# Kernel tuning notes

Hardware: AMD Instinct MI355X
Metric: run time of the kernel (lower is better)

The kernel has to match this reference:

```python
import jax, jax.numpy as jnp
import numpy as np

B, T, C, H = 2, 2048, 1024, 16
D = C // H  # head_dim = 64


def setup_inputs() -> dict:
    key = jax.random.key(0)
    ks = jax.random.split(key, 5)
    x = jax.random.normal(ks[0], (B, T, C), dtype=jnp.float32)
    # fused QKV projection: Linear(C, 3C)
    W_qkv = jax.random.normal(ks[1], (C, 3 * C), dtype=jnp.float32) / np.sqrt(C)
    b_qkv = jax.random.normal(ks[2], (3 * C,), dtype=jnp.float32) * 0.02
    # output projection: Linear(C, C)
    W_proj = jax.random.normal(ks[3], (C, C), dtype=jnp.float32) / np.sqrt(C)
    b_proj = jax.random.normal(ks[4], (C,), dtype=jnp.float32) * 0.02
    return {"x": x, "W_qkv": W_qkv, "b_qkv": b_qkv, "W_proj": W_proj, "b_proj": b_proj}


def reference(x, W_qkv, b_qkv, W_proj, b_proj):
    # fused QKV projection
    qkv = jnp.einsum("btc,cd->btd", x, W_qkv) + b_qkv  # [B,T,3C]
    q, k, v = jnp.split(qkv, 3, axis=-1)
    # [B,T,C] -> [B,H,T,D]
    def to_heads(t):
        return t.reshape(B, T, H, D).transpose(0, 2, 1, 3)
    q, k, v = to_heads(q), to_heads(k), to_heads(v)
    # causal scaled dot-product attention (SDPA default scale = 1/sqrt(head_dim))
    scale = 1.0 / np.sqrt(D).astype(np.float32)
    scores = jnp.einsum("bhqd,bhkd->bhqk", q, k) * scale  # [B,H,T,T]
    causal = jnp.tril(jnp.ones((T, T), dtype=bool))
    scores = jnp.where(causal, scores, jnp.finfo(scores.dtype).min)
    attn = jax.nn.softmax(scores, axis=-1)
    out = jnp.einsum("bhqk,bhkd->bhqd", attn, v)  # [B,H,T,D]
    out = out.transpose(0, 2, 1, 3).reshape(B, T, C)
    # output projection
    return jnp.einsum("btc,cd->btd", out, W_proj) + b_proj
```

## Files before the change

### kernel.cpp

```cpp
#include <hip/hip_runtime.h>
#include <hip/hip_bf16.h>

typedef __attribute__((ext_vector_type(8))) __bf16 bf16x8;
typedef __attribute__((ext_vector_type(8))) short short8;
typedef __attribute__((ext_vector_type(4))) float f32x4;
typedef __attribute__((ext_vector_type(16))) float f32x16;
typedef __attribute__((ext_vector_type(4))) short sh4;

typedef __attribute__((address_space(1))) void GVoid;
typedef __attribute__((address_space(3))) void LVoid;

#define NEGBIG (-1e30f)
#define SCL 0.18033688011112042f

constexpr int TT = 2048, CC = 1024, HH = 16, DD = 64, C3 = 3072;

__device__ __forceinline__ unsigned short f2bf(float f) {
  unsigned int i = __float_as_uint(f);
  return (unsigned short)((i + 0x7FFFu + ((i >> 16) & 1u)) >> 16);
}
__device__ __forceinline__ void async16(const void* g, void* l) {
  __builtin_amdgcn_global_load_lds((GVoid*)g, (LVoid*)l, 16, 0, 0);
}

__global__ __launch_bounds__(256) void cvt_bf16(
    const float* __restrict__ in, unsigned short* __restrict__ out, int n8)
{
  const int i = blockIdx.x * 256 + threadIdx.x;
  if (i >= n8) return;
  const float* p = in + (size_t)i * 8;
  f32x4 a = *(const f32x4*)p, b = *(const f32x4*)(p + 4);
  sh4 r0, r1;
  ((unsigned short*)&r0)[0] = f2bf(a[0]); ((unsigned short*)&r0)[1] = f2bf(a[1]);
  ((unsigned short*)&r0)[2] = f2bf(a[2]); ((unsigned short*)&r0)[3] = f2bf(a[3]);
  ((unsigned short*)&r1)[0] = f2bf(b[0]); ((unsigned short*)&r1)[1] = f2bf(b[1]);
  ((unsigned short*)&r1)[2] = f2bf(b[2]); ((unsigned short*)&r1)[3] = f2bf(b[3]);
  *(sh4*)(out + (size_t)i * 8) = r0;
  *(sh4*)(out + (size_t)i * 8 + 4) = r1;
}

__global__ __launch_bounds__(256) void transpose_cvt(
    const float* __restrict__ in, unsigned short* __restrict__ out, int R, int Cd)
{
  __shared__ __align__(16) unsigned short tile[64 * 72];
  const int r0 = blockIdx.y * 64, c0 = blockIdx.x * 64;
  const int tid = threadIdx.x;
#pragma unroll
  for (int r = 0; r < 2; ++r) {
    const int elem = r * 2048 + tid * 8;
    const int ii = elem >> 6, jj = elem & 63;
    const float* p = in + (size_t)(r0 + ii) * Cd + c0 + jj;
    f32x4 a = *(const f32x4*)p, b = *(const f32x4*)(p + 4);
    short8 v;
    ((unsigned short*)&v)[0] = f2bf(a[0]); ((unsigned short*)&v)[1] = f2bf(a[1]);
    ((unsigned short*)&v)[2] = f2bf(a[2]); ((unsigned short*)&v)[3] = f2bf(a[3]);
    ((unsigned short*)&v)[4] = f2bf(b[0]); ((unsigned short*)&v)[5] = f2bf(b[1]);
    ((unsigned short*)&v)[6] = f2bf(b[2]); ((unsigned short*)&v)[7] = f2bf(b[3]);
    *(short8*)&tile[ii * 72 + jj] = v;
  }
  __syncthreads();
#pragma unroll
  for (int r = 0; r < 2; ++r) {
    const int elem = r * 2048 + tid * 8;
    const int jj = elem >> 6, ii0 = elem & 63;
    short8 v;
#pragma unroll
    for (int e = 0; e < 8; ++e) ((unsigned short*)&v)[e] = tile[(ii0 + e) * 72 + jj];
    *(short8*)&out[(size_t)(c0 + jj) * R + r0 + ii0] = v;
  }
}

template <int MODE>
__global__ __launch_bounds__(256) void gemm_bt(
    const unsigned short* __restrict__ A,
    const unsigned short* __restrict__ Bt,
    const float* __restrict__ bias,
    void* __restrict__ Cp, unsigned short* __restrict__ Vt,
    int M, int N, int K, int lda)
{
  __shared__ __align__(16) unsigned short sA[2][128 * 32];
  __shared__ __align__(16) unsigned short sB[2][128 * 32];
  const int tid = threadIdx.x;
  const int w = tid >> 6, l = tid & 63, ln = l & 15, quad = l >> 4;
  const int wm = w >> 1, wn = w & 1;
  const int m0 = blockIdx.y * 128, n0 = blockIdx.x * 128;
  f32x4 acc[4][4] = {};

  const int elem0 = tid * 8;
  const int ar0 = elem0 >> 5, ac0 = elem0 & 31;
  const int ar1 = (2048 + elem0) >> 5, ac1 = ac0;

  async16(A  + (size_t)(m0 + ar0) * lda + ac0, &sA[0][w * 512]);
  async16(Bt + (size_t)(n0 + ar0) * K   + ac0, &sB[0][w * 512]);
  async16(A  + (size_t)(m0 + ar1) * lda + ac1, &sA[0][2048 + w * 512]);
  async16(Bt + (size_t)(n0 + ar1) * K   + ac1, &sB[0][2048 + w * 512]);
  __syncthreads();

  int buf = 0;
  for (int k0 = 0; k0 < K; k0 += 32, buf ^= 1) {
    if (k0 + 32 < K) {
      const int nb = buf ^ 1, kn = k0 + 32;
      async16(A  + (size_t)(m0 + ar0) * lda + kn + ac0, &sA[nb][w * 512]);
      async16(Bt + (size_t)(n0 + ar0) * K   + kn + ac0, &sB[nb][w * 512]);
      async16(A  + (size_t)(m0 + ar1) * lda + kn + ac1, &sA[nb][2048 + w * 512]);
      async16(Bt + (size_t)(n0 + ar1) * K   + kn + ac1, &sB[nb][2048 + w * 512]);
    }

    bf16x8 af[4], bfr[4];
#pragma unroll
    for (int i = 0; i < 4; i++)
      af[i] = *(const bf16x8*)&sA[buf][(wm * 64 + i * 16 + ln) * 32 + quad * 8];
#pragma unroll
    for (int j = 0; j < 4; j++)
      bfr[j] = *(const bf16x8*)&sB[buf][(wn * 64 + j * 16 + ln) * 32 + quad * 8];
#pragma unroll
    for (int i = 0; i < 4; i++)
#pragma unroll
      for (int j = 0; j < 4; j++)
        acc[i][j] = __builtin_amdgcn_mfma_f32_16x16x32_bf16(af[i], bfr[j], acc[i][j], 0, 0, 0);

    __syncthreads();
  }

  float bj[4];
#pragma unroll
  for (int j = 0; j < 4; j++) bj[j] = bias[n0 + wn * 64 + j * 16 + ln];

#pragma unroll
  for (int i = 0; i < 4; i++) {
#pragma unroll
    for (int j = 0; j < 4; j++) {
      const int gn = n0 + wn * 64 + j * 16 + ln;
      if (MODE == 0 && gn >= 2048) {
        const int hh = (gn >> 6) & 15, dd = gn & 63;
        const int gm0 = m0 + wm * 64 + i * 16 + quad * 4;
        const int bb = gm0 >> 11, t0 = gm0 & 2047;
        sh4 rv;
#pragma unroll
        for (int g = 0; g < 4; ++g)
          ((unsigned short*)&rv)[g] = f2bf(acc[i][j][g] + bj[j]);
        *(sh4*)&Vt[((size_t)((bb * HH + hh) * DD + dd)) * TT + t0] = rv;
      } else {
#pragma unroll
        for (int g = 0; g < 4; ++g) {
          const int gm = m0 + wm * 64 + i * 16 + quad * 4 + g;
          float v = acc[i][j][g] + bj[j];
          if (MODE == 0) {
            if (gn < 1024) v *= SCL;
            ((unsigned short*)Cp)[(size_t)gm * 2048 + gn] = f2bf(v);
          } else {
            ((float*)Cp)[(size_t)gm * N + gn] = v;
          }
        }
      }
    }
  }
}

__global__ __launch_bounds__(256) void gemm_n64(
    const unsigned short* __restrict__ A,
    const unsigned short* __restrict__ Bt,
    const float* __restrict__ bias,
    float* __restrict__ Cp, int M, int N, int K, int lda)
{
  __shared__ __align__(16) unsigned short sA[2][128 * 32];
  __shared__ __align__(16) unsigned short sB[2][64 * 32];
  const int tid = threadIdx.x;
  const int w = tid >> 6, l = tid & 63, ln = l & 15, quad = l >> 4;
  const int wm = w >> 1, wn = w & 1;
  const int m0 = blockIdx.y * 128, n0 = blockIdx.x * 64;
  f32x4 acc[4][2] = {};

  const int elem0 = tid * 8;
  const int ar0 = elem0 >> 5, ac0 = elem0 & 31;
  const int ar1 = (2048 + elem0) >> 5, ac1 = ac0;

  async16(A  + (size_t)(m0 + ar0) * lda + ac0, &sA[0][w * 512]);
  async16(A  + (size_t)(m0 + ar1) * lda + ac1, &sA[0][2048 + w * 512]);
  async16(Bt + (size_t)(n0 + ar0) * K   + ac0, &sB[0][w * 512]);
  __syncthreads();

  int buf = 0;
  for (int k0 = 0; k0 < K; k0 += 32, buf ^= 1) {
    if (k0 + 32 < K) {
      const int nb = buf ^ 1, kn = k0 + 32;
      async16(A  + (size_t)(m0 + ar0) * lda + kn + ac0, &sA[nb][w * 512]);
      async16(A  + (size_t)(m0 + ar1) * lda + kn + ac1, &sA[nb][2048 + w * 512]);
      async16(Bt + (size_t)(n0 + ar0) * K   + kn + ac0, &sB[nb][w * 512]);
    }

    bf16x8 af[4], bfr[2];
#pragma unroll
    for (int i = 0; i < 4; i++)
      af[i] = *(const bf16x8*)&sA[buf][(wm * 64 + i * 16 + ln) * 32 + quad * 8];
#pragma unroll
    for (int j = 0; j < 2; j++)
      bfr[j] = *(const bf16x8*)&sB[buf][(wn * 32 + j * 16 + ln) * 32 + quad * 8];
#pragma unroll
    for (int i = 0; i < 4; i++)
#pragma unroll
      for (int j = 0; j < 2; j++)
        acc[i][j] = __builtin_amdgcn_mfma_f32_16x16x32_bf16(af[i], bfr[j], acc[i][j], 0, 0, 0);

    __syncthreads();
  }

  float bj[2];
#pragma unroll
  for (int j = 0; j < 2; j++) bj[j] = bias[n0 + wn * 32 + j * 16 + ln];

#pragma unroll
  for (int i = 0; i < 4; i++)
#pragma unroll
    for (int g = 0; g < 4; ++g) {
      const int gm = m0 + wm * 64 + i * 16 + quad * 4 + g;
#pragma unroll
      for (int j = 0; j < 2; j++) {
        const int gn = n0 + wn * 32 + j * 16 + ln;
        Cp[(size_t)gm * N + gn] = acc[i][j][g] + bj[j];
      }
    }
}

__global__ __launch_bounds__(512) void attn2g(
    unsigned short* __restrict__ QK, const unsigned short* __restrict__ Vt)
{
  __shared__ __align__(16) unsigned short kt[2][2][64 * 72];
  __shared__ __align__(16) unsigned short vt[2][3][64 * 72];
  __shared__ float Ox[4][2][16][64];
  __shared__ float Lx[4][64];
  const int pair = blockIdx.x, bh = blockIdx.y;
  const int b = bh >> 4, h = bh & 15;
  const int tid = threadIdx.x;
  const int grp = tid >> 8, gtid = tid & 255;
  const int wg = (tid >> 6) & 3, l = tid & 63;
  const int c = l & 31, h2 = l >> 5;
  unsigned short*       Qp = QK + (size_t)b * TT * 2048 + h * DD;
  const unsigned short* Kp = QK + (size_t)b * TT * 2048 + CC + h * DD;
  const unsigned short* Vh = Vt + (size_t)bh * DD * TT;
  const int si0 = gtid >> 3, so = (gtid & 7) * 8;

  for (int ph = 0; ph < 2; ++ph) {
    const int qt = ph ? 15 - pair : pair;
    const int qbase = qt * 128 + wg * 32;
    const int qm = qbase + c - 4 * h2;
    bf16x8 qv[4];
#pragma unroll
    for (int ds = 0; ds < 4; ++ds)
      qv[ds] = *(const bf16x8*)&Qp[(size_t)(qbase + c) * 2048 + ds * 16 + h2 * 8];

    f32x16 oacc[2] = {};
    bf16x8 pA[4] = {};
    float lsum = 0.0f;
    const int nslot = qt + 1;
    int vm1 = 2, v0 = 0, vp1 = 1;

    __syncthreads();
#pragma unroll
    for (int r = 0; r < 2; ++r) {
      const int si = si0 + 32 * r;
      *(short8*)&kt[grp][0][si * 72 + so] =
          *(const short8*)&Kp[(size_t)(grp * 64 + si) * 2048 + so];
      *(short8*)&vt[grp][0][si * 72 + so] =
          *(const short8*)&Vh[(size_t)si * TT + grp * 64 + so];
    }
    __syncthreads();

    for (int slot = 0; slot < nslot; ++slot) {
      const int kb = 2 * slot + grp;
      const int ck = slot & 1;
      short8 pk[2], pv[2];
      if (slot + 1 < nslot) {
        const int kbn = kb + 2;
#pragma unroll
        for (int r = 0; r < 2; ++r) {
          const int si = si0 + 32 * r;
          pk[r] = *(const short8*)&Kp[(size_t)(kbn * 64 + si) * 2048 + so];
          pv[r] = *(const short8*)&Vh[(size_t)si * TT + kbn * 64 + so];
        }
      }
      const bool qk_act = (kb * 64 <= qbase + 31);
      f32x16 sacc[2];
      if (qk_act) {
#pragma unroll
        for (int kg = 0; kg < 2; ++kg) {
          f32x16 sa = {};
#pragma unroll
          for (int ds = 0; ds < 4; ++ds) {
            bf16x8 kf = *(const bf16x8*)&kt[grp][ck][(kg * 32 + c) * 72 + ds * 16 + h2 * 8];
            sa = __builtin_amdgcn_mfma_f32_32x32x16_bf16(kf, qv[ds], sa, 0, 0, 0);
          }
          sacc[kg] = sa;
        }
      }
      if (slot > 0 && (kb - 2) * 64 <= qbase + 31) {
        const unsigned short* vp = vt[grp][vm1];
#pragma unroll
        for (int dg = 0; dg < 2; ++dg)
#pragma unroll
          for (int ks = 0; ks < 4; ++ks) {
            bf16x8 vf = *(const bf16x8*)&vp[(dg * 32 + c) * 72 + ks * 16 + h2 * 8];
            oacc[dg] = __builtin_amdgcn_mfma_f32_32x32x16_bf16(pA[ks], vf, oacc[dg], 0, 0, 0);
          }
      }
      if (qk_act) {
        const bool need_mask = (kb * 64 + 63 > qbase);
        float pe[2][16];
#pragma unroll
        for (int kg = 0; kg < 2; ++kg)
#pragma unroll
          for (int rr = 0; rr < 16; ++rr) {
            float sv = sacc[kg][rr];
            if (need_mask) {
              const int krel = kb * 64 + kg * 32 + (rr & 3) + 8 * (rr >> 2);
              if (krel > qm) sv = NEGBIG;
            }
            float e;
            asm("v_exp_f32 %0, %1" : "=v"(e) : "v"(sv));
            pe[kg][rr] = e;
            lsum += e;
          }
        unsigned W0[2][4], W1[2][4];
#pragma unroll
        for (int kg = 0; kg < 2; ++kg)
#pragma unroll
          for (int r4 = 0; r4 < 4; ++r4) {
            asm("v_cvt_pk_bf16_f32 %0, %1, %2"
                : "=v"(W0[kg][r4]) : "v"(pe[kg][4 * r4 + 0]), "v"(pe[kg][4 * r4 + 1]));
            asm("v_cvt_pk_bf16_f32 %0, %1, %2"
                : "=v"(W1[kg][r4]) : "v"(pe[kg][4 * r4 + 2]), "v"(pe[kg][4 * r4 + 3]));
          }
#pragma unroll
        for (int ks = 0; ks < 4; ++ks) {
          const int kg = ks >> 1, sel = ks & 1;
          unsigned a0 = W0[kg][2 * sel], b0 = W0[kg][2 * sel + 1];
          unsigned a1 = W1[kg][2 * sel], b1 = W1[kg][2 * sel + 1];
          asm("v_permlane32_swap_b32 %0, %1" : "+v"(a0), "+v"(b0));
          asm("v_permlane32_swap_b32 %0, %1" : "+v"(a1), "+v"(b1));
          unsigned wds[4] = {a0, a1, b0, b1};
          pA[ks] = *(const bf16x8*)wds;
        }
      }
      if (slot + 1 < nslot) {
#pragma unroll
        for (int r = 0; r < 2; ++r) {
          const int si = si0 + 32 * r;
          *(short8*)&kt[grp][1 - ck][si * 72 + so] = pk[r];
          *(short8*)&vt[grp][vp1][si * 72 + so] = pv[r];
        }
      }
      __syncthreads();
      const int t_ = vm1; vm1 = v0; v0 = vp1; vp1 = t_;
    }
    const int kb_last = 2 * qt + grp;
    if (kb_last * 64 <= qbase + 31) {
      const unsigned short* vp = vt[grp][vm1];
#pragma unroll
      for (int dg = 0; dg < 2; ++dg)
#pragma unroll
        for (int ks = 0; ks < 4; ++ks) {
          bf16x8 vf = *(const bf16x8*)&vp[(dg * 32 + c) * 72 + ks * 16 + h2 * 8];
          oacc[dg] = __builtin_amdgcn_mfma_f32_32x32x16_bf16(pA[ks], vf, oacc[dg], 0, 0, 0);
        }
    }
    lsum += __shfl_xor(lsum, 32);
    if (grp == 1) {
#pragma unroll
      for (int dg = 0; dg < 2; ++dg)
#pragma unroll
        for (int rr = 0; rr < 16; ++rr) Ox[wg][dg][rr][l] = oacc[dg][rr];
      Lx[wg][l] = lsum;
    }
    __syncthreads();
    if (grp == 0) {
      const float inv = 1.0f / (lsum + Lx[wg][l]);
#pragma unroll
      for (int dg = 0; dg < 2; ++dg)
#pragma unroll
        for (int rr = 0; rr < 16; ++rr) oacc[dg][rr] += Ox[wg][dg][rr][l];
#pragma unroll
      for (int rr = 0; rr < 16; ++rr) {
        const int q_rel = (rr & 3) + 8 * (rr >> 2) + 4 * h2;
        const float iq = __shfl(inv, q_rel);
        const size_t trow = qbase + q_rel;
#pragma unroll
        for (int dg = 0; dg < 2; ++dg)
          Qp[trow * 2048 + dg * 32 + c] = f2bf(oacc[dg][rr] * iq);
      }
    }
  }
}

extern "C" void kernel_launch(void* const* d_in, const int* in_sizes, int n_in,
                              void* d_out, int out_size, void* d_ws, size_t ws_size,
                              hipStream_t stream)
{
  (void)in_sizes; (void)n_in; (void)out_size; (void)ws_size;
  const float* x     = (const float*)d_in[0];
  const float* Wqkv  = (const float*)d_in[1];
  const float* bqkv  = (const float*)d_in[2];
  const float* Wproj = (const float*)d_in[3];
  const float* bproj = (const float*)d_in[4];

  unsigned short* QK     = (unsigned short*)d_ws;
  unsigned short* WqkvT  = QK + (size_t)4096 * 2048;
  unsigned short* WprojT = WqkvT;
  unsigned short* Vt = (unsigned short*)d_out;
  unsigned short* xb = Vt + (size_t)32 * 64 * 2048;

  cvt_bf16<<<dim3(4096 * 1024 / 8 / 256), 256, 0, stream>>>(x, xb, 4096 * 1024 / 8);
  transpose_cvt<<<dim3(C3 / 64, CC / 64), 256, 0, stream>>>(Wqkv, WqkvT, CC, C3);
  gemm_bt<0><<<dim3(C3 / 128, 4096 / 128), 256, 0, stream>>>(
      xb, WqkvT, bqkv, QK, Vt, 4096, C3, CC, CC);
  transpose_cvt<<<dim3(CC / 64, CC / 64), 256, 0, stream>>>(Wproj, WprojT, CC, CC);
  attn2g<<<dim3(8, 2 * HH), 512, 0, stream>>>(QK, Vt);
  gemm_n64<<<dim3(CC / 64, 4096 / 128), 256, 0, stream>>>(
      QK, WprojT, bproj, (float*)d_out, 4096, CC, CC, 2048);
}
```

Before: 180.4 us.

## Split attention key blocks across four wave groups and swizzle GEMM block order

The attention kernel now runs 1024 threads per block, with four groups of waves each handling every fourth key block. Each group keeps its own double-buffered K/V tiles, replacing the two-group scheme that used a triple-buffered, software-pipelined P·V step. Partial outputs and row sums are reduced through shared memory that reuses the K/V buffers. Both GEMMs also remap block IDs with an 8-way swizzle, intended to improve L2 locality. The change adds more parallelism per attention tile, but costs a larger shared-memory footprint, only one block per CU, and a bigger final reduction.

```diff
diff --git a/kernel.cpp b/kernel.cpp
--- a/kernel.cpp
+++ b/kernel.cpp
@@ -83,7 +83,11 @@
   const int tid = threadIdx.x;
   const int w = tid >> 6, l = tid & 63, ln = l & 15, quad = l >> 4;
   const int wm = w >> 1, wn = w & 1;
-  const int m0 = blockIdx.y * 128, n0 = blockIdx.x * 128;
+  const int lid = blockIdx.y * gridDim.x + blockIdx.x;
+  const int per = (gridDim.x * gridDim.y) >> 3;
+  const int swz = (lid & 7) * per + (lid >> 3);
+  const int bx = swz / gridDim.y, by = swz % gridDim.y;
+  const int m0 = by * 128, n0 = bx * 128;
   f32x4 acc[4][4] = {};
 
   const int elem0 = tid * 8;
@@ -168,7 +172,11 @@
   const int tid = threadIdx.x;
   const int w = tid >> 6, l = tid & 63, ln = l & 15, quad = l >> 4;
   const int wm = w >> 1, wn = w & 1;
-  const int m0 = blockIdx.y * 128, n0 = blockIdx.x * 64;
+  const int lid = blockIdx.y * gridDim.x + blockIdx.x;
+  const int per = (gridDim.x * gridDim.y) >> 3;
+  const int swz = (lid & 7) * per + (lid >> 3);
+  const int bx = swz / gridDim.y, by = swz % gridDim.y;
+  const int m0 = by * 128, n0 = bx * 64;
   f32x4 acc[4][2] = {};
 
   const int elem0 = tid * 8;
@@ -222,23 +230,24 @@
     }
 }
 
-__global__ __launch_bounds__(512) void attn2g(
+__global__ __launch_bounds__(1024, 1) void attn4g(
     unsigned short* __restrict__ QK, const unsigned short* __restrict__ Vt)
 {
-  __shared__ __align__(16) unsigned short kt[2][2][64 * 72];
-  __shared__ __align__(16) unsigned short vt[2][3][64 * 72];
-  __shared__ float Ox[4][2][16][64];
-  __shared__ float Lx[4][64];
+  __shared__ __align__(16) unsigned short smem[73728];
   const int pair = blockIdx.x, bh = blockIdx.y;
   const int b = bh >> 4, h = bh & 15;
   const int tid = threadIdx.x;
-  const int grp = tid >> 8, gtid = tid & 255;
-  const int wg = (tid >> 6) & 3, l = tid & 63;
+  const int wid = tid >> 6, grp = wid >> 2, wg = wid & 3, l = tid & 63;
   const int c = l & 31, h2 = l >> 5;
+  const int gtid = tid & 255;
   unsigned short*       Qp = QK + (size_t)b * TT * 2048 + h * DD;
   const unsigned short* Kp = QK + (size_t)b * TT * 2048 + CC + h * DD;
   const unsigned short* Vh = Vt + (size_t)bh * DD * TT;
   const int si0 = gtid >> 3, so = (gtid & 7) * 8;
+  unsigned short* kt0 = smem + grp * 2 * 4608;
+  unsigned short* vt0 = smem + 36864 + grp * 2 * 4608;
+  float* Ms  = (float*)smem;
+  float* Lxp = (float*)smem + 24576;
 
   for (int ph = 0; ph < 2; ++ph) {
     const int qt = ph ? 15 - pair : pair;
@@ -250,60 +259,47 @@
       qv[ds] = *(const bf16x8*)&Qp[(size_t)(qbase + c) * 2048 + ds * 16 + h2 * 8];
 
     f32x16 oacc[2] = {};
-    bf16x8 pA[4] = {};
     float lsum = 0.0f;
-    const int nslot = qt + 1;
-    int vm1 = 2, v0 = 0, vp1 = 1;
+    const int kbmax = 2 * qt + 1;
+    const int nslot = (qt + 2) >> 1;
 
     __syncthreads();
-#pragma unroll
-    for (int r = 0; r < 2; ++r) {
-      const int si = si0 + 32 * r;
-      *(short8*)&kt[grp][0][si * 72 + so] =
-          *(const short8*)&Kp[(size_t)(grp * 64 + si) * 2048 + so];
-      *(short8*)&vt[grp][0][si * 72 + so] =
-          *(const short8*)&Vh[(size_t)si * TT + grp * 64 + so];
+    if (grp <= kbmax) {
+#pragma unroll
+      for (int r = 0; r < 2; ++r) {
+        const int si = si0 + 32 * r;
+        *(short8*)&kt0[si * 72 + so] = *(const short8*)&Kp[(size_t)(grp * 64 + si) * 2048 + so];
+        *(short8*)&vt0[si * 72 + so] = *(const short8*)&Vh[(size_t)si * TT + grp * 64 + so];
+      }
     }
     __syncthreads();
 
     for (int slot = 0; slot < nslot; ++slot) {
-      const int kb = 2 * slot + grp;
+      const int kb = 4 * slot + grp;
       const int ck = slot & 1;
+      const bool pref = (kb + 4 <= kbmax);
       short8 pk[2], pv[2];
-      if (slot + 1 < nslot) {
-        const int kbn = kb + 2;
+      if (pref) {
 #pragma unroll
         for (int r = 0; r < 2; ++r) {
           const int si = si0 + 32 * r;
-          pk[r] = *(const short8*)&Kp[(size_t)(kbn * 64 + si) * 2048 + so];
-          pv[r] = *(const short8*)&Vh[(size_t)si * TT + kbn * 64 + so];
-        }
-      }
-      const bool qk_act = (kb * 64 <= qbase + 31);
-      f32x16 sacc[2];
-      if (qk_act) {
+          pk[r] = *(const short8*)&Kp[(size_t)((kb + 4) * 64 + si) * 2048 + so];
+          pv[r] = *(const short8*)&Vh[(size_t)si * TT + (kb + 4) * 64 + so];
+        }
+      }
+      const bool act = (kb * 64 <= qbase + 31);
+      if (act) {
+        f32x16 sacc[2];
 #pragma unroll
         for (int kg = 0; kg < 2; ++kg) {
           f32x16 sa = {};
 #pragma unroll
           for (int ds = 0; ds < 4; ++ds) {
-            bf16x8 kf = *(const bf16x8*)&kt[grp][ck][(kg * 32 + c) * 72 + ds * 16 + h2 * 8];
+            bf16x8 kf = *(const bf16x8*)&kt0[ck * 4608 + (kg * 32 + c) * 72 + ds * 16 + h2 * 8];
             sa = __builtin_amdgcn_mfma_f32_32x32x16_bf16(kf, qv[ds], sa, 0, 0, 0);
           }
           sacc[kg] = sa;
         }
-      }
-      if (slot > 0 && (kb - 2) * 64 <= qbase + 31) {
-        const unsigned short* vp = vt[grp][vm1];
-#pragma unroll
-        for (int dg = 0; dg < 2; ++dg)
-#pragma unroll
-          for (int ks = 0; ks < 4; ++ks) {
-            bf16x8 vf = *(const bf16x8*)&vp[(dg * 32 + c) * 72 + ks * 16 + h2 * 8];
-            oacc[dg] = __builtin_amdgcn_mfma_f32_32x32x16_bf16(pA[ks], vf, oacc[dg], 0, 0, 0);
-          }
-      }
-      if (qk_act) {
         const bool need_mask = (kb * 64 + 63 > qbase);
         float pe[2][16];
 #pragma unroll
@@ -330,6 +326,7 @@
             asm("v_cvt_pk_bf16_f32 %0, %1, %2"
                 : "=v"(W1[kg][r4]) : "v"(pe[kg][4 * r4 + 2]), "v"(pe[kg][4 * r4 + 3]));
           }
+        bf16x8 pA[4];
 #pragma unroll
         for (int ks = 0; ks < 4; ++ks) {
           const int kg = ks >> 1, sel = ks & 1;
@@ -340,44 +337,50 @@
           unsigned wds[4] = {a0, a1, b0, b1};
           pA[ks] = *(const bf16x8*)wds;
         }
-      }
-      if (slot + 1 < nslot) {
+#pragma unroll
+        for (int dg = 0; dg < 2; ++dg)
+#pragma unroll
+          for (int ks = 0; ks < 4; ++ks) {
+            bf16x8 vf = *(const bf16x8*)&vt0[ck * 4608 + (dg * 32 + c) * 72 + ks * 16 + h2 * 8];
+            oacc[dg] = __builtin_amdgcn_mfma_f32_32x32x16_bf16(pA[ks], vf, oacc[dg], 0, 0, 0);
+          }
+      }
+      if (pref) {
 #pragma unroll
         for (int r = 0; r < 2; ++r) {
           const int si = si0 + 32 * r;
-          *(short8*)&kt[grp][1 - ck][si * 72 + so] = pk[r];
-          *(short8*)&vt[grp][vp1][si * 72 + so] = pv[r];
+          *(short8*)&kt0[(1 - ck) * 4608 + si * 72 + so] = pk[r];
+          *(short8*)&vt0[(1 - ck) * 4608 + si * 72 + so] = pv[r];
         }
       }
       __syncthreads();
-      const int t_ = vm1; vm1 = v0; v0 = vp1; vp1 = t_;
-    }
-    const int kb_last = 2 * qt + grp;
-    if (kb_last * 64 <= qbase + 31) {
-      const unsigned short* vp = vt[grp][vm1];
+    }
+    lsum += __shfl_xor(lsum, 32);
+    if (grp != 0) {
+      const int base = ((grp - 1) * 4 + wg) * 2048;
 #pragma unroll
       for (int dg = 0; dg < 2; ++dg)
 #pragma unroll
-        for (int ks = 0; ks < 4; ++ks) {
-          bf16x8 vf = *(const bf16x8*)&vp[(dg * 32 + c) * 72 + ks * 16 + h2 * 8];
-          oacc[dg] = __builtin_amdgcn_mfma_f32_32x32x16_bf16(pA[ks], vf, oacc[dg], 0, 0, 0);
-        }
-    }
-    lsum += __shfl_xor(lsum, 32);
-    if (grp == 1) {
-#pragma unroll
-      for (int dg = 0; dg < 2; ++dg)
-#pragma unroll
-        for (int rr = 0; rr < 16; ++rr) Ox[wg][dg][rr][l] = oacc[dg][rr];
-      Lx[wg][l] = lsum;
+        for (int rr = 0; rr < 16; ++rr)
+          Ms[base + (dg * 16 + rr) * 64 + l] = oacc[dg][rr];
+      Lxp[((grp - 1) * 4 + wg) * 64 + l] = lsum;
     }
     __syncthreads();
     if (grp == 0) {
-      const float inv = 1.0f / (lsum + Lx[wg][l]);
+      float lt = lsum;
+#pragma unroll
+      for (int g = 1; g < 4; ++g) lt += Lxp[((g - 1) * 4 + wg) * 64 + l];
+      const float inv = 1.0f / lt;
 #pragma unroll
       for (int dg = 0; dg < 2; ++dg)
 #pragma unroll
-        for (int rr = 0; rr < 16; ++rr) oacc[dg][rr] += Ox[wg][dg][rr][l];
+        for (int rr = 0; rr < 16; ++rr) {
+          float o = oacc[dg][rr];
+#pragma unroll
+          for (int g = 1; g < 4; ++g)
+            o += Ms[((g - 1) * 4 + wg) * 2048 + (dg * 16 + rr) * 64 + l];
+          oacc[dg][rr] = o;
+        }
 #pragma unroll
       for (int rr = 0; rr < 16; ++rr) {
         const int q_rel = (rr & 3) + 8 * (rr >> 2) + 4 * h2;
@@ -413,7 +416,7 @@
   gemm_bt<0><<<dim3(C3 / 128, 4096 / 128), 256, 0, stream>>>(
       xb, WqkvT, bqkv, QK, Vt, 4096, C3, CC, CC);
   transpose_cvt<<<dim3(CC / 64, CC / 64), 256, 0, stream>>>(Wproj, WprojT, CC, CC);
-  attn2g<<<dim3(8, 2 * HH), 512, 0, stream>>>(QK, Vt);
+  attn4g<<<dim3(8, 2 * HH), 1024, 0, stream>>>(QK, Vt);
   gemm_n64<<<dim3(CC / 64, 4096 / 128), 256, 0, stream>>>(
       QK, WprojT, bproj, (float*)d_out, 4096, CC, CC, 2048);
 }
```

Measured after the change: 203.2 us. 1.13x slower.
